# Kernel optimization log

Measured on AMD Instinct MI355X. Metric: run time of the kernel, lower is better.

## Reference

```python
import jax, jax.numpy as jnp
import numpy as np

MARGIN = 0.1  # init kwarg margin
B, N = 16384, 50


def setup_inputs() -> dict:
    key = jax.random.key(0)
    k1, k2 = jax.random.split(key)
    scores = jax.random.normal(k1, (B * N,), dtype=jnp.float32)
    # per-segment permutation of [0, N): hypotheses ordered by WER
    werRank = jnp.argsort(jax.random.uniform(k2, (B, N)), axis=-1).astype(jnp.int32)
    return {"scores": scores, "werRank": werRank, "nBest": N}


def reference(scores, werRank, nBest):
    # scores: [B*N] flat concatenated nBest scores; werRank: [B,N] permutations.
    b = werRank.shape[0]
    seg = scores.reshape(b, nBest)                      # [B, N]
    ranked = jnp.take_along_axis(seg, werRank, axis=1)  # score at rank j, [B, N]
    # hinge[b, j, k] = relu(margin - (pos_j - neg_k))
    hinge = jnp.maximum(0.0, MARGIN - (ranked[:, :, None] - ranked[:, None, :]))
    j = jnp.arange(nBest)
    tri = (j[None, :] > j[:, None]).astype(scores.dtype)          # k > j mask, [N, N]
    counts = (nBest - 1 - j[:-1]).astype(scores.dtype)            # #neg per rank j
    # reduction='mean' over negatives for each j, then summed over j and batch
    per_j = (hinge * tri[None, :, :]).sum(-1)[:, :-1] / counts[None, :]  # [B, N-1]
    total = jnp.sum(per_j)
    return total.reshape(1)
```

## Files before the change

kernel.cpp:

```cpp
#include <hip/hip_runtime.h>

#define NBEST 50
#define MARGIN 0.1f
#define WAVES_PER_BLOCK 4
#define SEGS_PER_WAVE 4
#define SEGS_PER_BLOCK (WAVES_PER_BLOCK * SEGS_PER_WAVE)
#define GRID_BLOCKS 1024
#define TAG 0x5A5A5A5Au

typedef unsigned long long u64;

__global__ void __launch_bounds__(256)
margin_onenode_kernel(const float* __restrict__ scores,
                      const int* __restrict__ werRank,
                      u64* __restrict__ parts,
                      float* __restrict__ out, int B) {
    const int wave = threadIdx.x >> 6;
    const int lane = threadIdx.x & 63;

    __shared__ float r[WAVES_PER_BLOCK][64];
    __shared__ float wsum[WAVES_PER_BLOCK];

    const float recip = (lane < NBEST - 1) ? 1.0f / (float)(NBEST - 1 - lane) : 0.0f;

    const int seg0 = (blockIdx.x * WAVES_PER_BLOCK + wave) * SEGS_PER_WAVE;
    float vsum = 0.0f;

    #pragma unroll
    for (int i = 0; i < SEGS_PER_WAVE; ++i) {
        const int seg = seg0 + i;
        float s = 0.0f;
        int   wr = 0;
        if (seg < B && lane < NBEST) {
            const int base = seg * NBEST;
            s  = scores[base + lane];
            wr = werRank[base + lane];
        }
        const float rj = __shfl(s, wr, 64);
        r[wave][lane] = rj;

        const float c = MARGIN - rj;
        float acc_j = 0.0f;
        #pragma unroll
        for (int k = 1; k < NBEST; ++k) {
            const float d = fmaxf(c + r[wave][k], 0.0f);
            acc_j += (lane < k) ? d : 0.0f;
        }
        vsum += acc_j * recip;
    }

    #pragma unroll
    for (int off = 32; off >= 1; off >>= 1)
        vsum += __shfl_xor(vsum, off, 64);

    if (lane == 0) wsum[wave] = vsum;
    __syncthreads();

    if (threadIdx.x == 0) {
        float t = 0.0f;
        #pragma unroll
        for (int w = 0; w < WAVES_PER_BLOCK; ++w) t += wsum[w];
        const unsigned int b = __float_as_uint(t);
        const u64 pk = (u64)b | ((u64)(b ^ TAG) << 32);
        __hip_atomic_store(&parts[blockIdx.x], pk,
                           __ATOMIC_RELAXED, __HIP_MEMORY_SCOPE_AGENT);
    }

    if (blockIdx.x != 0) return;

    __syncthreads();

    float s = 0.0f;
    {
        unsigned int bits[4];
        for (;;) {
            bool ok = true;
            #pragma unroll
            for (int q = 0; q < 4; ++q) {
                const u64 pk = __hip_atomic_load(
                    &parts[threadIdx.x + 256 * q],
                    __ATOMIC_RELAXED, __HIP_MEMORY_SCOPE_AGENT);
                bits[q] = (unsigned int)pk;
                ok &= ((unsigned int)(pk >> 32) == (bits[q] ^ TAG));
            }
            if (ok) break;
            __builtin_amdgcn_s_sleep(1);
        }
        #pragma unroll
        for (int q = 0; q < 4; ++q)
            s += __uint_as_float(bits[q]);
    }
    #pragma unroll
    for (int off = 32; off >= 1; off >>= 1)
        s += __shfl_xor(s, off, 64);
    if (lane == 0) wsum[wave] = s;
    __syncthreads();
    if (threadIdx.x == 0) {
        float total = 0.0f;
        #pragma unroll
        for (int w = 0; w < WAVES_PER_BLOCK; ++w) total += wsum[w];
        out[0] = total;
    }
}

extern "C" void kernel_launch(void* const* d_in, const int* in_sizes, int n_in,
                              void* d_out, int out_size, void* d_ws, size_t ws_size,
                              hipStream_t stream) {
    const float* scores  = (const float*)d_in[0];
    const int*   werRank = (const int*)d_in[1];
    float*       out     = (float*)d_out;
    u64*         parts   = (u64*)d_ws;

    const int B = in_sizes[0] / NBEST;

    margin_onenode_kernel<<<GRID_BLOCKS, WAVES_PER_BLOCK * 64, 0, stream>>>(
        scores, werRank, parts, out, B);
}
```

Before: 15.51 us.

## Use 1024-thread blocks over 256 blocks, shrink final cross-block reduction

Raises each block from 4 to 16 waves and cuts the grid from 1024 to 256 blocks. Each thread of block 0 now polls a single partial instead of four, so the final spin-wait and reduction get shorter. The segment bounds check and the B argument are removed, which hardcodes the assumption that B equals 256*16*4 segments. Larger blocks may lower scheduling flexibility, and block 0 must still wait for every other block to finish.

```diff
diff --git a/kernel.cpp b/kernel.cpp
--- a/kernel.cpp
+++ b/kernel.cpp
@@ -2,19 +2,19 @@
 
 #define NBEST 50
 #define MARGIN 0.1f
-#define WAVES_PER_BLOCK 4
+#define WAVES_PER_BLOCK 16
 #define SEGS_PER_WAVE 4
 #define SEGS_PER_BLOCK (WAVES_PER_BLOCK * SEGS_PER_WAVE)
-#define GRID_BLOCKS 1024
+#define GRID_BLOCKS 256
 #define TAG 0x5A5A5A5Au
 
 typedef unsigned long long u64;
 
-__global__ void __launch_bounds__(256)
+__global__ void __launch_bounds__(1024)
 margin_onenode_kernel(const float* __restrict__ scores,
                       const int* __restrict__ werRank,
                       u64* __restrict__ parts,
-                      float* __restrict__ out, int B) {
+                      float* __restrict__ out) {
     const int wave = threadIdx.x >> 6;
     const int lane = threadIdx.x & 63;
 
@@ -31,7 +31,7 @@
         const int seg = seg0 + i;
         float s = 0.0f;
         int   wr = 0;
-        if (seg < B && lane < NBEST) {
+        if (lane < NBEST) {
             const int base = seg * NBEST;
             s  = scores[base + lane];
             wr = werRank[base + lane];
@@ -70,30 +70,24 @@
 
     __syncthreads();
 
-    float s = 0.0f;
-    {
-        unsigned int bits[4];
+    float v = 0.0f;
+    if (threadIdx.x < GRID_BLOCKS) {
         for (;;) {
-            bool ok = true;
-            #pragma unroll
-            for (int q = 0; q < 4; ++q) {
-                const u64 pk = __hip_atomic_load(
-                    &parts[threadIdx.x + 256 * q],
-                    __ATOMIC_RELAXED, __HIP_MEMORY_SCOPE_AGENT);
-                bits[q] = (unsigned int)pk;
-                ok &= ((unsigned int)(pk >> 32) == (bits[q] ^ TAG));
+            const u64 pk = __hip_atomic_load(&parts[threadIdx.x],
+                                             __ATOMIC_RELAXED,
+                                             __HIP_MEMORY_SCOPE_AGENT);
+            const unsigned int lo = (unsigned int)pk;
+            if ((unsigned int)(pk >> 32) == (lo ^ TAG)) {
+                v = __uint_as_float(lo);
+                break;
             }
-            if (ok) break;
             __builtin_amdgcn_s_sleep(1);
         }
-        #pragma unroll
-        for (int q = 0; q < 4; ++q)
-            s += __uint_as_float(bits[q]);
     }
     #pragma unroll
     for (int off = 32; off >= 1; off >>= 1)
-        s += __shfl_xor(s, off, 64);
-    if (lane == 0) wsum[wave] = s;
+        v += __shfl_xor(v, off, 64);
+    if (lane == 0) wsum[wave] = v;
     __syncthreads();
     if (threadIdx.x == 0) {
         float total = 0.0f;
@@ -111,8 +105,6 @@
     float*       out     = (float*)d_out;
     u64*         parts   = (u64*)d_ws;
 
-    const int B = in_sizes[0] / NBEST;
-
     margin_onenode_kernel<<<GRID_BLOCKS, WAVES_PER_BLOCK * 64, 0, stream>>>(
-        scores, werRank, parts, out, B);
+        scores, werRank, parts, out);
 }
```

Result: slower. 22.66 us (+46.2%).
